# Kernel tuning notes

Measured on AMD Instinct MI355X. Metric: run time of the kernel, lower is better.

## Reference

```python
import jax, jax.numpy as jnp
import numpy as np


def setup_inputs() -> dict:
    key = jax.random.key(0)
    ks = jax.random.split(key, 6)
    B, H, N, C, O, G = 4, 24, 512, 120, 512, 5
    x = jax.random.normal(ks[0], (B, H, N, C), dtype=jnp.float32)
    t_indices = jnp.arange(H, dtype=jnp.int64)
    time_emb = jax.random.normal(ks[1], (H, 8), dtype=jnp.float32)
    # kaiming-uniform-ish init for base linear weight
    fan_in = C + 8
    bound = float(np.sqrt(6.0 / fan_in))
    base_w = jax.random.uniform(ks[2], (O, C + 8), minval=-bound, maxval=bound, dtype=jnp.float32)
    base_b = jax.random.uniform(ks[3], (O,), minval=-1.0 / np.sqrt(fan_in), maxval=1.0 / np.sqrt(fan_in), dtype=jnp.float32)
    spline_weight = jax.random.uniform(ks[4], (O, C + 8, G), minval=-0.1, maxval=0.1, dtype=jnp.float32)
    return {"x": x, "t_indices": t_indices, "time_emb": time_emb,
            "base_w": base_w, "base_b": base_b, "spline_weight": spline_weight}


def reference(x, t_indices, time_emb, base_w, base_b, spline_weight):
    B, H, N, C = x.shape
    G = spline_weight.shape[-1]
    grid = jnp.linspace(-1.0, 1.0, G, dtype=x.dtype)  # non-trainable buffer
    # time embedding lookup, broadcast over batch and nodes: [B,H,N,8]
    t_emb = jnp.broadcast_to(time_emb[t_indices][None, :, None, :], (B, H, N, time_emb.shape[-1]))
    x_in = jnp.concatenate([x, t_emb], axis=-1)  # [B,H,N,C+8]
    # base path: SiLU then linear
    base = jnp.einsum('bhni,oi->bhno', jax.nn.silu(x_in), base_w) + base_b
    # RBF basis: [B,H,N,C+8,G]
    inv_h = (G - 1) / 2.0  # 1 / (2/(G-1))
    basis = jnp.exp(-(((x_in[..., None] - grid) * inv_h) ** 2))
    spline = jnp.einsum('bhnig,oig->bhno', basis, spline_weight)
    return base + spline
```

## Files before the change

kernel.cpp:

```cpp
#include <hip/hip_runtime.h>
#include <hip/hip_bf16.h>

typedef __attribute__((ext_vector_type(4))) float f32x4;
typedef __attribute__((ext_vector_type(8))) short bf16x8;

#define GLDS16(gp, lp) __builtin_amdgcn_global_load_lds( \
    (__attribute__((address_space(1))) void*)(void*)(gp), \
    (__attribute__((address_space(3))) void*)(lp), 16, 0, 0)

static constexpr int Mtot = 49152;
static constexpr int Otot = 512;
static constexpr int Hh   = 24;

__device__ inline unsigned short f2bf(float f) {
    __hip_bfloat16 h = __float2bfloat16(f);
    unsigned short u;
    __builtin_memcpy(&u, &h, 2);
    return u;
}

__device__ inline uint4 gen8(const int f, const float4 a, const float4 b) {
    float v[8] = {a.x, a.y, a.z, a.w, b.x, b.y, b.z, b.w};
    unsigned short s[8];
    if (f == 0) {
        #pragma unroll
        for (int e = 0; e < 8; ++e)
            s[e] = f2bf(v[e] * __builtin_amdgcn_rcpf(1.0f + __expf(-v[e])));
    } else {
        const float cg = -1.0f + 0.5f * (float)(f - 1);
        #pragma unroll
        for (int e = 0; e < 8; ++e) {
            const float d = 2.0f * (v[e] - cg);
            s[e] = f2bf(__expf(-d * d));
        }
    }
    uint4 u;
    u.x = s[0] | ((unsigned)s[1] << 16);
    u.y = s[2] | ((unsigned)s[3] << 16);
    u.z = s[4] | ((unsigned)s[5] << 16);
    u.w = s[6] | ((unsigned)s[7] << 16);
    return u;
}

__global__ __launch_bounds__(256) void prep_W(
        const float* __restrict__ bw, const float* __restrict__ sw,
        uint4* __restrict__ Wt)
{
    const int tid = blockIdx.x * 256 + threadIdx.x;
    const int col = tid & 511;
    const int C   = tid >> 9;
    const int f   = C >> 4;
    const int i0  = (C & 15) * 8;
    unsigned short s[8];
    if (f == 0) {
        const float4 a = *(const float4*)(bw + col * 128 + i0);
        const float4 b = *(const float4*)(bw + col * 128 + i0 + 4);
        const float v[8] = {a.x, a.y, a.z, a.w, b.x, b.y, b.z, b.w};
        #pragma unroll
        for (int e = 0; e < 8; ++e) s[e] = f2bf(v[e]);
    } else {
        #pragma unroll
        for (int e = 0; e < 8; ++e)
            s[e] = f2bf(sw[(col * 128 + i0 + e) * 5 + (f - 1)]);
    }
    uint4 u;
    u.x = s[0] | ((unsigned)s[1] << 16);
    u.y = s[2] | ((unsigned)s[3] << 16);
    u.z = s[4] | ((unsigned)s[5] << 16);
    u.w = s[6] | ((unsigned)s[7] << 16);
    Wt[tid] = u;
}

__global__ __launch_bounds__(512, 2) void gemm_kan(
        const float* __restrict__ x, const int* __restrict__ t_idx,
        const float* __restrict__ temb,
        const char* __restrict__ Wt,
        const float* __restrict__ bias,
        float* __restrict__ out)
{
    __shared__ char Alds[8 * 128 * 16];
    __shared__ char Blds[2][8 * 512 * 16];

    const int t    = threadIdx.x;
    const int wave = t >> 6;
    const int lane = t & 63;
    const int ll   = lane & 15;
    const int q4   = lane >> 4;
    const int wm   = (wave >> 2) * 64;
    const int wn   = (wave & 3) * 128;
    const int m_base = blockIdx.x * 128;

    const int row = t >> 2;
    const int cp  = t & 3;
    const int ht  = t_idx[(m_base >> 9) % Hh];
    const float* xrow = x + (size_t)(m_base + row) * 120;
    const float* trow = temb + ht * 8;

    float4 xc[4][2];
    #pragma unroll
    for (int g = 0; g < 4; ++g) {
        const int i0 = ((g & 1) * 8 + cp + (g >> 1) * 4) * 8;
        const float* p = (i0 < 120) ? (xrow + i0) : (trow + (i0 - 120));
        xc[g][0] = *(const float4*)p;
        xc[g][1] = *(const float4*)(p + 4);
    }

    f32x4 acc[4][8] = {};

    auto stageB = [&](int it, int buf) {
        const char* src = Wt + ((size_t)((it * 8 + wave) * 512 + lane) << 4);
        char* dst = &Blds[buf][wave * 8192];
        #pragma unroll
        for (int q = 0; q < 8; ++q)
            GLDS16(src + (q << 10), dst + (q << 10));
    };

    stageB(0, 0);
    {
        uint4 a0 = gen8(0, xc[0][0], xc[0][1]);
        uint4 a1 = gen8(0, xc[2][0], xc[2][1]);
        *(uint4*)(Alds + (((cp    ) * 128 + row) << 4)) = a0;
        *(uint4*)(Alds + (((cp + 4) * 128 + row) << 4)) = a1;
    }
    uint4 p0 = gen8(0, xc[1][0], xc[1][1]);
    uint4 p1 = gen8(0, xc[3][0], xc[3][1]);
    __syncthreads();

    #pragma unroll
    for (int it = 0; it < 12; ++it) {
        if (it + 1 < 12) stageB(it + 1, (it + 1) & 1);

        uint4 n0 = {}, n1 = {};
        if (it + 2 < 12) {
            const int f = (it + 2) >> 1, h = (it + 2) & 1;
            n0 = gen8(f, xc[h][0],     xc[h][1]);
            n1 = gen8(f, xc[2 + h][0], xc[2 + h][1]);
        }

        const char* B = Blds[it & 1];
        #pragma unroll
        for (int kk = 0; kk < 2; ++kk) {
            const int ch = kk * 4 + q4;
            bf16x8 af[4], bf[8];
            #pragma unroll
            for (int mi = 0; mi < 4; ++mi)
                af[mi] = *(const bf16x8*)(Alds + ((ch * 128 + wm + mi * 16 + ll) << 4));
            #pragma unroll
            for (int ni = 0; ni < 8; ++ni)
                bf[ni] = *(const bf16x8*)(B + ((ch * 512 + wn + ni * 16 + ll) << 4));
            #pragma unroll
            for (int mi = 0; mi < 4; ++mi)
                #pragma unroll
                for (int ni = 0; ni < 8; ++ni)
                    acc[mi][ni] = __builtin_amdgcn_mfma_f32_16x16x32_bf16(
                        af[mi], bf[ni], acc[mi][ni], 0, 0, 0);
        }
        __syncthreads();
        if (it + 1 < 12) {
            *(uint4*)(Alds + (((cp    ) * 128 + row) << 4)) = p0;
            *(uint4*)(Alds + (((cp + 4) * 128 + row) << 4)) = p1;
            p0 = n0; p1 = n1;
        }
        __syncthreads();
    }

    const int col0 = wn + ll;
    const int row0 = m_base + wm + q4 * 4;
    #pragma unroll
    for (int ni = 0; ni < 8; ++ni) {
        const int col = col0 + ni * 16;
        const float bv = bias[col];
        #pragma unroll
        for (int mi = 0; mi < 4; ++mi) {
            #pragma unroll
            for (int r = 0; r < 4; ++r) {
                out[(size_t)(row0 + mi * 16 + r) * Otot + col] = acc[mi][ni][r] + bv;
            }
        }
    }
}

extern "C" void kernel_launch(void* const* d_in, const int* in_sizes, int n_in,
                              void* d_out, int out_size, void* d_ws, size_t ws_size,
                              hipStream_t stream) {
    const float* x    = (const float*)d_in[0];
    const int*   tidx = (const int*)  d_in[1];
    const float* temb = (const float*)d_in[2];
    const float* bw   = (const float*)d_in[3];
    const float* bb   = (const float*)d_in[4];
    const float* sw   = (const float*)d_in[5];
    float* out = (float*)d_out;

    char* Wt = (char*)d_ws;

    prep_W<<<49152 / 256, 256, 0, stream>>>(bw, sw, (uint4*)Wt);
    gemm_kan<<<Mtot / 128, 512, 0, stream>>>(x, tidx, temb, Wt, bb, out);
}
```

Measured before the change: 180.3 us.

## Split N across two blocks with 256 threads and regenerate A tiles per iteration

```diff
diff --git a/kernel.cpp b/kernel.cpp
--- a/kernel.cpp
+++ b/kernel.cpp
@@ -19,15 +19,15 @@
     return u;
 }
 
-__device__ inline uint4 gen8(const int f, const float4 a, const float4 b) {
+__device__ inline uint4 gen8(const bool silu, const float cg,
+                             const float4 a, const float4 b) {
     float v[8] = {a.x, a.y, a.z, a.w, b.x, b.y, b.z, b.w};
     unsigned short s[8];
-    if (f == 0) {
+    if (silu) {
         #pragma unroll
         for (int e = 0; e < 8; ++e)
             s[e] = f2bf(v[e] * __builtin_amdgcn_rcpf(1.0f + __expf(-v[e])));
     } else {
-        const float cg = -1.0f + 0.5f * (float)(f - 1);
         #pragma unroll
         for (int e = 0; e < 8; ++e) {
             const float d = 2.0f * (v[e] - cg);
@@ -71,7 +71,7 @@
     Wt[tid] = u;
 }
 
-__global__ __launch_bounds__(512, 2) void gemm_kan(
+__global__ __launch_bounds__(256, 2) void gemm_kan(
         const float* __restrict__ x, const int* __restrict__ t_idx,
         const float* __restrict__ temb,
         const char* __restrict__ Wt,
@@ -79,63 +79,72 @@
         float* __restrict__ out)
 {
     __shared__ char Alds[8 * 128 * 16];
-    __shared__ char Blds[2][8 * 512 * 16];
+    __shared__ char Blds[2][8 * 256 * 16];
 
     const int t    = threadIdx.x;
     const int wave = t >> 6;
     const int lane = t & 63;
     const int ll   = lane & 15;
     const int q4   = lane >> 4;
-    const int wm   = (wave >> 2) * 64;
-    const int wn   = (wave & 3) * 128;
-    const int m_base = blockIdx.x * 128;
-
-    const int row = t >> 2;
-    const int cp  = t & 3;
+    const int wm   = (wave >> 1) * 64;
+    const int wn   = (wave & 1) * 128;
+
+    const int bid  = blockIdx.x;
+    const int swz  = (bid & 7) * 96 + (bid >> 3);
+    const int m_base = (swz >> 1) * 128;
+    const int n_base = (swz & 1) * 256;
+
+    const int row = t >> 1;
+    const int hh  = t & 1;
     const int ht  = t_idx[(m_base >> 9) % Hh];
     const float* xrow = x + (size_t)(m_base + row) * 120;
     const float* trow = temb + ht * 8;
 
-    float4 xc[4][2];
-    #pragma unroll
-    for (int g = 0; g < 4; ++g) {
-        const int i0 = ((g & 1) * 8 + cp + (g >> 1) * 4) * 8;
-        const float* p = (i0 < 120) ? (xrow + i0) : (trow + (i0 - 120));
-        xc[g][0] = *(const float4*)p;
-        xc[g][1] = *(const float4*)(p + 4);
-    }
-
     f32x4 acc[4][8] = {};
 
     auto stageB = [&](int it, int buf) {
-        const char* src = Wt + ((size_t)((it * 8 + wave) * 512 + lane) << 4);
-        char* dst = &Blds[buf][wave * 8192];
-        #pragma unroll
-        for (int q = 0; q < 8; ++q)
-            GLDS16(src + (q << 10), dst + (q << 10));
+        #pragma unroll
+        for (int q = 0; q < 8; ++q) {
+            const int c = 2 * wave + (q >> 2);
+            const char* src = Wt + (((size_t)(it * 8 + c) * 512 + n_base) << 4)
+                              + (q & 3) * 1024 + lane * 16;
+            GLDS16(src, Blds[buf] + c * 4096 + (q & 3) * 1024);
+        }
     };
 
+    auto chanptr = [&](int c0) -> const float* {
+        return (c0 < 120) ? (xrow + c0) : (trow + (c0 - 120));
+    };
+
+    float4 pa, pb;
+    {
+        const float* p = chanptr(hh * 32);
+        pa = *(const float4*)p;
+        pb = *(const float4*)(p + 4);
+    }
+
     stageB(0, 0);
-    {
-        uint4 a0 = gen8(0, xc[0][0], xc[0][1]);
-        uint4 a1 = gen8(0, xc[2][0], xc[2][1]);
-        *(uint4*)(Alds + (((cp    ) * 128 + row) << 4)) = a0;
-        *(uint4*)(Alds + (((cp + 4) * 128 + row) << 4)) = a1;
-    }
-    uint4 p0 = gen8(0, xc[1][0], xc[1][1]);
-    uint4 p1 = gen8(0, xc[3][0], xc[3][1]);
-    __syncthreads();
-
-    #pragma unroll
+
+    #pragma unroll 2
     for (int it = 0; it < 12; ++it) {
+        const int  half = it & 1;
+        const bool silu = (it < 2);
+        const float cg  = -1.0f + 0.5f * (float)((it >> 1) - 1);
+
+        #pragma unroll
+        for (int j = 0; j < 4; ++j) {
+            const float4 fa = pa, fb = pb;
+            const int jn = (j + 1) & 3;
+            const int hn = (j == 3) ? (half ^ 1) : half;
+            const float* p = chanptr(hn * 64 + hh * 32 + jn * 8);
+            pa = *(const float4*)p;
+            pb = *(const float4*)(p + 4);
+            const uint4 u = gen8(silu, cg, fa, fb);
+            *(uint4*)(Alds + (((hh * 4 + j) * 128 + row) << 4)) = u;
+        }
+        __syncthreads();
+
         if (it + 1 < 12) stageB(it + 1, (it + 1) & 1);
-
-        uint4 n0 = {}, n1 = {};
-        if (it + 2 < 12) {
-            const int f = (it + 2) >> 1, h = (it + 2) & 1;
-            n0 = gen8(f, xc[h][0],     xc[h][1]);
-            n1 = gen8(f, xc[2 + h][0], xc[2 + h][1]);
-        }
 
         const char* B = Blds[it & 1];
         #pragma unroll
@@ -147,7 +156,7 @@
                 af[mi] = *(const bf16x8*)(Alds + ((ch * 128 + wm + mi * 16 + ll) << 4));
             #pragma unroll
             for (int ni = 0; ni < 8; ++ni)
-                bf[ni] = *(const bf16x8*)(B + ((ch * 512 + wn + ni * 16 + ll) << 4));
+                bf[ni] = *(const bf16x8*)(B + ((ch * 256 + wn + ni * 16 + ll) << 4));
             #pragma unroll
             for (int mi = 0; mi < 4; ++mi)
                 #pragma unroll
@@ -156,15 +165,9 @@
                         af[mi], bf[ni], acc[mi][ni], 0, 0, 0);
         }
         __syncthreads();
-        if (it + 1 < 12) {
-            *(uint4*)(Alds + (((cp    ) * 128 + row) << 4)) = p0;
-            *(uint4*)(Alds + (((cp + 4) * 128 + row) << 4)) = p1;
-            p0 = n0; p1 = n1;
-        }
-        __syncthreads();
-    }
-
-    const int col0 = wn + ll;
+    }
+
+    const int col0 = n_base + wn + ll;
     const int row0 = m_base + wm + q4 * 4;
     #pragma unroll
     for (int ni = 0; ni < 8; ++ni) {
@@ -194,5 +197,5 @@
     char* Wt = (char*)d_ws;
 
     prep_W<<<49152 / 256, 256, 0, stream>>>(bw, sw, (uint4*)Wt);
-    gemm_kan<<<Mtot / 128, 512, 0, stream>>>(x, tidx, temb, Wt, bb, out);
-}
+    gemm_kan<<<768, 256, 0, stream>>>(x, tidx, temb, Wt, bb, out);
+}
```

Measured after the change: 212.8 us. 18.0% more time.
